# Performance work log

Hardware: AMD Instinct MI355X
Metric: run time of the kernel (lower is better)

## Reference

```python
import jax, jax.numpy as jnp
import numpy as np

B, T, C, H = 4, 2048, 1024, 16
HD = C // H  # head dim = 64


def setup_inputs() -> dict:
    key = jax.random.key(0)
    k1, k2, k3 = jax.random.split(key, 3)
    x = jax.random.normal(k1, (B, T, C), dtype=jnp.float32)
    # nn.Linear weight init scale ~ 1/sqrt(fan_in); keep magnitudes sane
    w_qkv = jax.random.normal(k2, (C, 3 * C), dtype=jnp.float32) * (1.0 / np.sqrt(C))
    w_out = jax.random.normal(k3, (C, C), dtype=jnp.float32) * (1.0 / np.sqrt(C))
    return {"x": x, "w_qkv": w_qkv, "w_out": w_out}


def _attention(x, w_qkv, w_out):
    Bs, Ts, Cs = x.shape
    qkv = x @ w_qkv                                  # [B,T,3C]
    q, k, v = jnp.split(qkv, 3, axis=-1)
    # [B,T,C] -> [B,H,T,hd]
    def heads(t):
        return t.reshape(Bs, Ts, H, HD).transpose(0, 2, 1, 3)
    q, k, v = heads(q), heads(k), heads(v)
    scale = 1.0 / np.sqrt(HD)
    scores = jnp.einsum("bhqd,bhkd->bhqk", q, k) * scale  # [B,H,T,T]
    causal = jnp.tril(jnp.ones((Ts, Ts), dtype=bool))
    scores = jnp.where(causal, scores, jnp.finfo(scores.dtype).min)
    probs = jax.nn.softmax(scores, axis=-1)
    attn = jnp.einsum("bhqk,bhkd->bhqd", probs, v)        # [B,H,T,hd]
    attn = attn.transpose(0, 2, 1, 3).reshape(Bs, Ts, Cs)  # [B,T,C]
    return attn @ w_out  # dropout_p=0 at eval


def reference(x, w_qkv, w_out):
    return _attention(x, w_qkv, w_out)
```

## Files before the change

kernel.cpp:

```cpp
#include <hip/hip_runtime.h>
#include <hip/hip_bf16.h>

#define B_   4
#define T_   2048
#define C_   1024
#define H_   16
#define HD_  64
#define BH_  (B_*H_)
#define M_   (B_*T_)
#define N1_  (3*C_)

typedef __hip_bfloat16 bf16;
typedef __attribute__((ext_vector_type(8))) __bf16 bf16x8v;
typedef __attribute__((ext_vector_type(4))) float  f32x4;

#define QSCALE 0.18033688f

__device__ __forceinline__ f32x4 mfma16(bf16x8v a, bf16x8v b, f32x4 c) {
    return __builtin_amdgcn_mfma_f32_16x16x32_bf16(a, b, c, 0, 0, 0);
}

__device__ __forceinline__ float exp2_hw(float x) {
    return __builtin_amdgcn_exp2f(x);
}

typedef __attribute__((address_space(3))) unsigned int       lds_u32;
typedef const __attribute__((address_space(1))) unsigned int glb_u32;
__device__ __forceinline__ void async16(void* lds, const void* g) {
    __builtin_amdgcn_global_load_lds((glb_u32*)g, (lds_u32*)lds, 16, 0, 0);
}

__global__ void convert_f32_bf16(const float* __restrict__ in, bf16* __restrict__ out) {
    const int i = blockIdx.x * blockDim.x + threadIdx.x;
    float f[8];
    *(float4*)(f)     = ((const float4*)in)[i*2];
    *(float4*)(f + 4) = ((const float4*)in)[i*2 + 1];
    bf16 t[8];
#pragma unroll
    for (int j = 0; j < 8; ++j) t[j] = __float2bfloat16(f[j]);
    ((uint4*)out)[i] = *(uint4*)t;
}

__global__ void transpose_f32_to_bf16(const float* __restrict__ in,
                                      bf16* __restrict__ out, int K, int N) {
    __shared__ float t[32][33];
    const int n0 = blockIdx.x * 32, k0 = blockIdx.y * 32;
    const int c  = threadIdx.x & 31;
    const int rr = threadIdx.x >> 5;
#pragma unroll
    for (int i = 0; i < 4; ++i)
        t[c][rr + 8*i] = in[(size_t)(k0 + rr + 8*i) * N + n0 + c];
    __syncthreads();
#pragma unroll
    for (int i = 0; i < 4; ++i)
        out[(size_t)(n0 + rr + 8*i) * K + k0 + c] = __float2bfloat16(t[rr + 8*i][c]);
}

template<int EPI>
__global__ __launch_bounds__(256, 2)
void gemm_lds(const bf16* __restrict__ A, const bf16* __restrict__ Bt,
              float* __restrict__ Cmat, int N, int K,
              bf16* __restrict__ qb, bf16* __restrict__ kb, bf16* __restrict__ vb)
{
    __shared__ bf16 Alds[128][64];
    __shared__ bf16 Blds[128][64];

    const int tid  = threadIdx.x;
    const int wave = tid >> 6, lane = tid & 63;
    const int quad = lane >> 4, l16 = lane & 15;
    const int wm   = (wave >> 1) * 64, wn = (wave & 1) * 64;
    const size_t row0 = (size_t)blockIdx.y * 128;
    const size_t col0 = (size_t)blockIdx.x * 128;

    const f32x4 z4 = {0.f, 0.f, 0.f, 0.f};
    f32x4 acc[4][4];
#pragma unroll
    for (int mi = 0; mi < 4; ++mi)
#pragma unroll
        for (int ni = 0; ni < 4; ++ni) acc[mi][ni] = z4;

    const int grow = lane >> 3;
    const int gcol = ((lane & 7) ^ (lane >> 3)) * 8;
    const bf16* pA = A  + (row0 + wave*32 + grow) * (size_t)K + gcol;
    const bf16* pB = Bt + (col0 + wave*32 + grow) * (size_t)K + gcol;
    bf16* lA = &Alds[wave*32][0];
    bf16* lB = &Blds[wave*32][0];

    const int fsw = (l16 & 7);

    for (int k0 = 0; k0 < K; k0 += 64) {
#pragma unroll
        for (int j = 0; j < 4; ++j)
            async16(lA + j*512, pA + (size_t)j*8*K + k0);
#pragma unroll
        for (int j = 0; j < 4; ++j)
            async16(lB + j*512, pB + (size_t)j*8*K + k0);
        __syncthreads();

#pragma unroll
        for (int kp = 0; kp < 2; ++kp) {
            const int fg = ((kp*4 + quad) ^ fsw) * 8;
            bf16x8v af[4], bfr[4];
#pragma unroll
            for (int i = 0; i < 4; ++i) {
                af[i]  = *(const bf16x8v*)(&Alds[wm + i*16 + l16][fg]);
                bfr[i] = *(const bf16x8v*)(&Blds[wn + i*16 + l16][fg]);
            }
#pragma unroll
            for (int mi = 0; mi < 4; ++mi)
#pragma unroll
                for (int ni = 0; ni < 4; ++ni)
                    acc[mi][ni] = mfma16(af[mi], bfr[ni], acc[mi][ni]);
        }
        __syncthreads();
    }

#pragma unroll
    for (int mi = 0; mi < 4; ++mi) {
        const size_t rowb = row0 + wm + mi*16 + quad*4;
#pragma unroll
        for (int ni = 0; ni < 4; ++ni) {
            const size_t col = col0 + wn + ni*16 + l16;
#pragma unroll
            for (int r = 0; r < 4; ++r) {
                const float v = acc[mi][ni][r];
                if constexpr (EPI == 0) {
                    Cmat[(rowb + r) * N + col] = v;
                } else {
                    const int rowi = (int)(rowb + r);
                    const int b  = rowi >> 11;
                    const int t  = rowi & (T_ - 1);
                    const int coli = (int)col;
                    const int type = coli >> 10;
                    const int cc2  = coli & (C_ - 1);
                    const int h = cc2 >> 6, d = cc2 & (HD_ - 1);
                    const int bh = b * H_ + h;
                    if (type == 0)
                        qb[((size_t)bh * T_ + t) * HD_ + d] = __float2bfloat16(v * QSCALE);
                    else if (type == 1)
                        kb[((size_t)bh * T_ + t) * HD_ + d] = __float2bfloat16(v);
                    else
                        vb[((size_t)bh * HD_ + d) * T_ + t] = __float2bfloat16(v);
                }
            }
        }
    }
}

#define KP 72
#define VP 72

__global__ __launch_bounds__(256, 3)
void attn_pair(const bf16* __restrict__ qb, const bf16* __restrict__ kb,
               const bf16* __restrict__ vb, bf16* __restrict__ attn)
{
    __shared__ bf16 Klds[2][64][KP];
    __shared__ bf16 Vlds[2][64][VP];
    __shared__ float Llds[4][2][16];

    const int tid  = threadIdx.x;
    const int wave = tid >> 6, lane = tid & 63;
    const int quad = lane >> 4, l16 = lane & 15;
    const int bh   = blockIdx.y;

    const bf16* Q  = qb + (size_t)bh * T_ * HD_;
    const bf16* Kp = kb + (size_t)bh * T_ * HD_;
    const bf16* Vp = vb + (size_t)bh * HD_ * T_;

    const int kr = tid >> 3;
    const int kc = (tid & 7) * 8;

    const int b = bh >> 4, h = bh & (H_ - 1);
    const f32x4 z4 = {0.f, 0.f, 0.f, 0.f};

    const int krow_base = ((l16 >> 2) * 8) + (l16 & 3);

    const int tiles[2] = { (int)blockIdx.x, 15 - (int)blockIdx.x };

    uint4 kreg0 = *(const uint4*)(Kp + (size_t)kr        * HD_ + kc);
    uint4 kreg1 = *(const uint4*)(Kp + (size_t)(kr + 32) * HD_ + kc);
    uint4 vreg0 = *(const uint4*)(Vp + (size_t)kr        * T_  + kc);
    uint4 vreg1 = *(const uint4*)(Vp + (size_t)(kr + 32) * T_  + kc);

    int p = 0;

#pragma unroll 1
    for (int tt = 0; tt < 2; ++tt) {
        const int q0b = tiles[tt] * 128;
        const int q0w = q0b + wave * 32;

        bf16x8v qf[2][2];
#pragma unroll
        for (int nq = 0; nq < 2; ++nq)
#pragma unroll
            for (int kp = 0; kp < 2; ++kp)
                qf[nq][kp] = *(const bf16x8v*)(Q + (size_t)(q0w + nq*16 + l16) * HD_ + kp*32 + quad*8);

        f32x4 o[2][4];
#pragma unroll
        for (int nq = 0; nq < 2; ++nq)
#pragma unroll
            for (int di = 0; di < 4; ++di) o[nq][di] = z4;
        float l_nq[2] = {0.f, 0.f};

        const int kend = q0b + 128;

#pragma unroll 1
        for (int k0 = 0; k0 < kend; k0 += 64) {
            *(uint4*)(&Klds[p][kr][kc])      = kreg0;
            *(uint4*)(&Klds[p][kr + 32][kc]) = kreg1;
            *(uint4*)(&Vlds[p][kr][kc])      = vreg0;
            *(uint4*)(&Vlds[p][kr + 32][kc]) = vreg1;
            __syncthreads();

            const int kn = (k0 + 64 < kend) ? (k0 + 64) : 0;
            kreg0 = *(const uint4*)(Kp + (size_t)(kn + kr)      * HD_ + kc);
            kreg1 = *(const uint4*)(Kp + (size_t)(kn + kr + 32) * HD_ + kc);
            vreg0 = *(const uint4*)(Vp + (size_t)kr        * T_ + kn + kc);
            vreg1 = *(const uint4*)(Vp + (size_t)(kr + 32) * T_ + kn + kc);

            if (k0 <= q0w + 31) {
                f32x4 st[4][2];
#pragma unroll
                for (int mk = 0; mk < 4; ++mk)
#pragma unroll
                    for (int nq = 0; nq < 2; ++nq) st[mk][nq] = z4;
#pragma unroll
                for (int kp = 0; kp < 2; ++kp) {
                    bf16x8v kf[4];
#pragma unroll
                    for (int mk = 0; mk < 4; ++mk)
                        kf[mk] = *(const bf16x8v*)(&Klds[p][krow_base + (mk>>1)*32 + (mk&1)*4][kp*32 + quad*8]);
#pragma unroll
                    for (int mk = 0; mk < 4; ++mk) {
                        st[mk][0] = mfma16(kf[mk], qf[0][kp], st[mk][0]);
                        st[mk][1] = mfma16(kf[mk], qf[1][kp], st[mk][1]);
                    }
                }
                if (k0 + 63 > q0w) {
#pragma unroll
                    for (int mk = 0; mk < 4; ++mk) {
                        const int keyb = k0 + (mk>>1)*32 + quad*8 + (mk&1)*4;
#pragma unroll
                        for (int nq = 0; nq < 2; ++nq) {
                            const int qrow = q0w + nq*16 + l16;
#pragma unroll
                            for (int r = 0; r < 4; ++r)
                                if (keyb + r > qrow) st[mk][nq][r] = -3.0e38f;
                        }
                    }
                }
                bf16x8v pa[2][2];
#pragma unroll
                for (int nq = 0; nq < 2; ++nq) {
#pragma unroll
                    for (int kp = 0; kp < 2; ++kp) {
                        union { bf16x8v v; bf16 hh[8]; } u;
                        float sum = 0.f;
#pragma unroll
                        for (int jh = 0; jh < 2; ++jh) {
                            const int mk = kp*2 + jh;
#pragma unroll
                            for (int r = 0; r < 4; ++r) {
                                const float e = exp2_hw(st[mk][nq][r]);
                                sum += e;
                                u.hh[jh*4 + r] = __float2bfloat16(e);
                            }
                        }
                        l_nq[nq] += sum;
                        pa[nq][kp] = u.v;
                    }
                }
#pragma unroll
                for (int kp = 0; kp < 2; ++kp)
#pragma unroll
                    for (int di = 0; di < 4; ++di) {
                        const bf16x8v vf = *(const bf16x8v*)(&Vlds[p][di*16 + l16][kp*32 + quad*8]);
                        o[0][di] = mfma16(pa[0][kp], vf, o[0][di]);
                        o[1][di] = mfma16(pa[1][kp], vf, o[1][di]);
                    }
            }
            p ^= 1;
        }

#pragma unroll
        for (int nq = 0; nq < 2; ++nq) {
            float l = l_nq[nq];
            l += __shfl_xor(l, 16);
            l += __shfl_xor(l, 32);
            if (quad == 0) Llds[wave][nq][l16] = l;
        }
#pragma unroll
        for (int nq = 0; nq < 2; ++nq) {
            const f32x4 lv = *(const f32x4*)(&Llds[wave][nq][quad*4]);
#pragma unroll
            for (int r = 0; r < 4; ++r) {
                const float inv = 1.0f / lv[r];
                const int t = q0w + nq*16 + quad*4 + r;
                const size_t base = ((size_t)(b * T_ + t)) * C_ + h * HD_;
#pragma unroll
                for (int di = 0; di < 4; ++di)
                    attn[base + di*16 + l16] = __float2bfloat16(o[nq][di][r] * inv);
            }
        }
    }
}

extern "C" void kernel_launch(void* const* d_in, const int* in_sizes, int n_in,
                              void* d_out, int out_size, void* d_ws, size_t ws_size,
                              hipStream_t stream)
{
    const float* x     = (const float*)d_in[0];
    const float* w_qkv = (const float*)d_in[1];
    const float* w_out = (const float*)d_in[2];
    float* out = (float*)d_out;

    char* ws = (char*)d_ws;
    bf16* qb     = (bf16*)(ws);
    bf16* kb     = (bf16*)(ws + (size_t)16 * 1024 * 1024);
    bf16* vb     = (bf16*)(ws + (size_t)32 * 1024 * 1024);
    bf16* xb     = (bf16*)(ws + (size_t)48 * 1024 * 1024);
    bf16* attnb  = xb;
    bf16* wtqkv  = (bf16*)(ws + (size_t)64 * 1024 * 1024);
    bf16* wtout  = (bf16*)(ws + (size_t)70 * 1024 * 1024);

    convert_f32_bf16<<<dim3((M_*C_)/(8*256)), 256, 0, stream>>>(x, xb);

    transpose_f32_to_bf16<<<dim3(N1_/32, C_/32), 256, 0, stream>>>(w_qkv, wtqkv, C_, N1_);
    transpose_f32_to_bf16<<<dim3(C_/32,  C_/32), 256, 0, stream>>>(w_out, wtout, C_, C_);

    gemm_lds<1><<<dim3(N1_/128, M_/128), 256, 0, stream>>>(
        xb, wtqkv, nullptr, N1_, C_, qb, kb, vb);

    attn_pair<<<dim3(8, BH_), 256, 0, stream>>>(qb, kb, vb, attnb);

    gemm_lds<0><<<dim3(C_/128, M_/128), 256, 0, stream>>>(
        attnb, wtout, out, C_, C_, nullptr, nullptr, nullptr);
}
```

Measured before the change: 251.1 us.

## Split attention key range across two wave groups and fuse prep kernels

The attention kernel now uses 512 threads per block, with two groups of four waves each processing alternating 64-key chunks of the causal range for the same query tile. Partial outputs and row sums from the first group are merged through LDS by the second group before normalization and store. This doubles the waves working on each query tile to improve latency hiding and occupancy, at the cost of extra barriers and an LDS reduction. Separately, the input conversion and the two weight transposes are merged into one launch to cut launch overhead.

Result: slower. 263.3 us (+4.9%).

```diff
diff --git a/kernel.cpp b/kernel.cpp
--- a/kernel.cpp
+++ b/kernel.cpp
@@ -30,21 +30,28 @@
     __builtin_amdgcn_global_load_lds((glb_u32*)g, (lds_u32*)lds, 16, 0, 0);
 }
 
-__global__ void convert_f32_bf16(const float* __restrict__ in, bf16* __restrict__ out) {
-    const int i = blockIdx.x * blockDim.x + threadIdx.x;
-    float f[8];
-    *(float4*)(f)     = ((const float4*)in)[i*2];
-    *(float4*)(f + 4) = ((const float4*)in)[i*2 + 1];
-    bf16 t[8];
-#pragma unroll
-    for (int j = 0; j < 8; ++j) t[j] = __float2bfloat16(f[j]);
-    ((uint4*)out)[i] = *(uint4*)t;
-}
-
-__global__ void transpose_f32_to_bf16(const float* __restrict__ in,
-                                      bf16* __restrict__ out, int K, int N) {
+__global__ void prep(const float* __restrict__ x,  bf16* __restrict__ xb,
+                     const float* __restrict__ wq, bf16* __restrict__ wqt,
+                     const float* __restrict__ wo, bf16* __restrict__ wot)
+{
     __shared__ float t[32][33];
-    const int n0 = blockIdx.x * 32, k0 = blockIdx.y * 32;
+    const int bid = blockIdx.x;
+    if (bid < 4096) {
+        const int i = bid * 256 + threadIdx.x;
+        float f[8];
+        *(float4*)(f)     = ((const float4*)x)[(size_t)i*2];
+        *(float4*)(f + 4) = ((const float4*)x)[(size_t)i*2 + 1];
+        bf16 tb[8];
+#pragma unroll
+        for (int j = 0; j < 8; ++j) tb[j] = __float2bfloat16(f[j]);
+        ((uint4*)xb)[i] = *(uint4*)tb;
+        return;
+    }
+    const float* in; bf16* out; int K, N, n0, k0;
+    if (bid < 7168) { const int b2 = bid - 4096; in = wq; out = wqt; K = C_; N = N1_;
+                      n0 = (b2 % 96) * 32; k0 = (b2 / 96) * 32; }
+    else            { const int b2 = bid - 7168; in = wo; out = wot; K = C_; N = C_;
+                      n0 = (b2 % 32) * 32; k0 = (b2 / 32) * 32; }
     const int c  = threadIdx.x & 31;
     const int rr = threadIdx.x >> 5;
 #pragma unroll
@@ -86,7 +93,7 @@
     bf16* lA = &Alds[wave*32][0];
     bf16* lB = &Blds[wave*32][0];
 
-    const int fsw = (l16 & 7);
+    const int fsw = l16 & 7;
 
     for (int k0 = 0; k0 < K; k0 += 64) {
 #pragma unroll
@@ -147,19 +154,20 @@
     }
 }
 
-#define KP 72
-#define VP 72
-
-__global__ __launch_bounds__(256, 3)
-void attn_pair(const bf16* __restrict__ qb, const bf16* __restrict__ kb,
-               const bf16* __restrict__ vb, bf16* __restrict__ attn)
+#define KP2 72
+
+__global__ __launch_bounds__(512, 4)
+void attn_ks(const bf16* __restrict__ qb, const bf16* __restrict__ kb,
+             const bf16* __restrict__ vb, bf16* __restrict__ attn)
 {
-    __shared__ bf16 Klds[2][64][KP];
-    __shared__ bf16 Vlds[2][64][VP];
-    __shared__ float Llds[4][2][16];
+    __shared__ bf16 KV[2][2][2][64][KP2];
+    __shared__ float Ls0[4][2][16];
+    __shared__ float Lt[4][2][16];
+    float* Os = (float*)&KV[0][0][0][0][0];
 
     const int tid  = threadIdx.x;
     const int wave = tid >> 6, lane = tid & 63;
+    const int g    = wave >> 2, w2 = wave & 3;
     const int quad = lane >> 4, l16 = lane & 15;
     const int bh   = blockIdx.y;
 
@@ -167,27 +175,27 @@
     const bf16* Kp = kb + (size_t)bh * T_ * HD_;
     const bf16* Vp = vb + (size_t)bh * HD_ * T_;
 
-    const int kr = tid >> 3;
-    const int kc = (tid & 7) * 8;
+    const int ltid = tid & 255;
+    const int kr = ltid >> 3;
+    const int kc = (ltid & 7) * 8;
 
     const int b = bh >> 4, h = bh & (H_ - 1);
     const f32x4 z4 = {0.f, 0.f, 0.f, 0.f};
-
     const int krow_base = ((l16 >> 2) * 8) + (l16 & 3);
-
     const int tiles[2] = { (int)blockIdx.x, 15 - (int)blockIdx.x };
 
-    uint4 kreg0 = *(const uint4*)(Kp + (size_t)kr        * HD_ + kc);
-    uint4 kreg1 = *(const uint4*)(Kp + (size_t)(kr + 32) * HD_ + kc);
-    uint4 vreg0 = *(const uint4*)(Vp + (size_t)kr        * T_  + kc);
-    uint4 vreg1 = *(const uint4*)(Vp + (size_t)(kr + 32) * T_  + kc);
+    uint4 kreg0 = *(const uint4*)(Kp + (size_t)(g*64 + kr)      * HD_ + kc);
+    uint4 kreg1 = *(const uint4*)(Kp + (size_t)(g*64 + kr + 32) * HD_ + kc);
+    uint4 vreg0 = *(const uint4*)(Vp + (size_t)kr        * T_ + g*64 + kc);
+    uint4 vreg1 = *(const uint4*)(Vp + (size_t)(kr + 32) * T_ + g*64 + kc);
 
     int p = 0;
 
 #pragma unroll 1
     for (int tt = 0; tt < 2; ++tt) {
-        const int q0b = tiles[tt] * 128;
-        const int q0w = q0b + wave * 32;
+        const int ti  = tiles[tt];
+        const int q0b = ti * 128;
+        const int q0w = q0b + w2 * 32;
 
         bf16x8v qf[2][2];
 #pragma unroll
@@ -203,17 +211,18 @@
             for (int di = 0; di < 4; ++di) o[nq][di] = z4;
         float l_nq[2] = {0.f, 0.f};
 
-        const int kend = q0b + 128;
+        const int iters = ti + 1;
 
 #pragma unroll 1
-        for (int k0 = 0; k0 < kend; k0 += 64) {
-            *(uint4*)(&Klds[p][kr][kc])      = kreg0;
-            *(uint4*)(&Klds[p][kr + 32][kc]) = kreg1;
-            *(uint4*)(&Vlds[p][kr][kc])      = vreg0;
-            *(uint4*)(&Vlds[p][kr + 32][kc]) = vreg1;
+        for (int j = 0; j < iters; ++j) {
+            const int k0 = g*64 + j*128;
+            *(uint4*)(&KV[0][g][p][kr][kc])      = kreg0;
+            *(uint4*)(&KV[0][g][p][kr + 32][kc]) = kreg1;
+            *(uint4*)(&KV[1][g][p][kr][kc])      = vreg0;
+            *(uint4*)(&KV[1][g][p][kr + 32][kc]) = vreg1;
             __syncthreads();
 
-            const int kn = (k0 + 64 < kend) ? (k0 + 64) : 0;
+            const int kn = (j + 1 < iters) ? (k0 + 128) : (g*64);
             kreg0 = *(const uint4*)(Kp + (size_t)(kn + kr)      * HD_ + kc);
             kreg1 = *(const uint4*)(Kp + (size_t)(kn + kr + 32) * HD_ + kc);
             vreg0 = *(const uint4*)(Vp + (size_t)kr        * T_ + kn + kc);
@@ -230,7 +239,7 @@
                     bf16x8v kf[4];
 #pragma unroll
                     for (int mk = 0; mk < 4; ++mk)
-                        kf[mk] = *(const bf16x8v*)(&Klds[p][krow_base + (mk>>1)*32 + (mk&1)*4][kp*32 + quad*8]);
+                        kf[mk] = *(const bf16x8v*)(&KV[0][g][p][krow_base + (mk>>1)*32 + (mk&1)*4][kp*32 + quad*8]);
 #pragma unroll
                     for (int mk = 0; mk < 4; ++mk) {
                         st[mk][0] = mfma16(kf[mk], qf[0][kp], st[mk][0]);
@@ -275,7 +284,7 @@
                 for (int kp = 0; kp < 2; ++kp)
 #pragma unroll
                     for (int di = 0; di < 4; ++di) {
-                        const bf16x8v vf = *(const bf16x8v*)(&Vlds[p][di*16 + l16][kp*32 + quad*8]);
+                        const bf16x8v vf = *(const bf16x8v*)(&KV[1][g][p][di*16 + l16][kp*32 + quad*8]);
                         o[0][di] = mfma16(pa[0][kp], vf, o[0][di]);
                         o[1][di] = mfma16(pa[1][kp], vf, o[1][di]);
                     }
@@ -283,26 +292,52 @@
             p ^= 1;
         }
 
+        __syncthreads();
+        float lr[2];
 #pragma unroll
         for (int nq = 0; nq < 2; ++nq) {
             float l = l_nq[nq];
             l += __shfl_xor(l, 16);
             l += __shfl_xor(l, 32);
-            if (quad == 0) Llds[wave][nq][l16] = l;
-        }
-#pragma unroll
-        for (int nq = 0; nq < 2; ++nq) {
-            const f32x4 lv = *(const f32x4*)(&Llds[wave][nq][quad*4]);
-#pragma unroll
-            for (int r = 0; r < 4; ++r) {
-                const float inv = 1.0f / lv[r];
-                const int t = q0w + nq*16 + quad*4 + r;
-                const size_t base = ((size_t)(b * T_ + t)) * C_ + h * HD_;
-#pragma unroll
-                for (int di = 0; di < 4; ++di)
-                    attn[base + di*16 + l16] = __float2bfloat16(o[nq][di][r] * inv);
-            }
-        }
+            lr[nq] = l;
+        }
+        if (g == 0) {
+#pragma unroll
+            for (int nq = 0; nq < 2; ++nq) {
+                if (quad == 0) Ls0[w2][nq][l16] = lr[nq];
+#pragma unroll
+                for (int r = 0; r < 4; ++r) {
+                    const int row = w2*32 + nq*16 + quad*4 + r;
+#pragma unroll
+                    for (int di = 0; di < 4; ++di)
+                        Os[row*68 + di*16 + l16] = o[nq][di][r];
+                }
+            }
+        }
+        __syncthreads();
+        if (g == 1) {
+#pragma unroll
+            for (int nq = 0; nq < 2; ++nq) {
+                const float ltot = lr[nq] + Ls0[w2][nq][l16];
+                if (quad == 0) Lt[w2][nq][l16] = ltot;
+            }
+#pragma unroll
+            for (int nq = 0; nq < 2; ++nq) {
+                const f32x4 lv = *(const f32x4*)(&Lt[w2][nq][quad*4]);
+#pragma unroll
+                for (int r = 0; r < 4; ++r) {
+                    const float inv = 1.0f / lv[r];
+                    const int row = w2*32 + nq*16 + quad*4 + r;
+                    const int t = q0b + row;
+                    const size_t base = ((size_t)(b * T_ + t)) * C_ + h * HD_;
+#pragma unroll
+                    for (int di = 0; di < 4; ++di)
+                        attn[base + di*16 + l16] =
+                            __float2bfloat16((o[nq][di][r] + Os[row*68 + di*16 + l16]) * inv);
+                }
+            }
+        }
+        __syncthreads();
     }
 }
 
@@ -324,15 +359,12 @@
     bf16* wtqkv  = (bf16*)(ws + (size_t)64 * 1024 * 1024);
     bf16* wtout  = (bf16*)(ws + (size_t)70 * 1024 * 1024);
 
-    convert_f32_bf16<<<dim3((M_*C_)/(8*256)), 256, 0, stream>>>(x, xb);
-
-    transpose_f32_to_bf16<<<dim3(N1_/32, C_/32), 256, 0, stream>>>(w_qkv, wtqkv, C_, N1_);
-    transpose_f32_to_bf16<<<dim3(C_/32,  C_/32), 256, 0, stream>>>(w_out, wtout, C_, C_);
+    prep<<<dim3(8192), 256, 0, stream>>>(x, xb, w_qkv, wtqkv, w_out, wtout);
 
     gemm_lds<1><<<dim3(N1_/128, M_/128), 256, 0, stream>>>(
         xb, wtqkv, nullptr, N1_, C_, qb, kb, vb);
 
-    attn_pair<<<dim3(8, BH_), 256, 0, stream>>>(qb, kb, vb, attnb);
+    attn_ks<<<dim3(8, BH_), 512, 0, stream>>>(qb, kb, vb, attnb);
 
     gemm_lds<0><<<dim3(C_/128, M_/128), 256, 0, stream>>>(
         attnb, wtout, out, C_, C_, nullptr, nullptr, nullptr);
```
